# Performance work log

Measured on AMD Instinct MI355X. Metric: run time of the kernel, lower is better.

## Reference

```python
import jax, jax.numpy as jnp
import numpy as np

INV_SQRT2 = 0.7071067811865476  # pywt haar: cA=(x0+x1)/sqrt2, cD=(x0-x1)/sqrt2


def haar_dwt2(x):
    # x: (..., H, W) with even H, W. Matches pywt.dwt2 (cA, (cH, cV, cD))
    # keys: cH='da' (detail along rows), cV='ad', cD='dd'.
    aw = (x[..., ::2] + x[..., 1::2]) * INV_SQRT2   # low-pass along W
    dw = (x[..., ::2] - x[..., 1::2]) * INV_SQRT2   # high-pass along W
    LL = (aw[..., ::2, :] + aw[..., 1::2, :]) * INV_SQRT2
    LH = (aw[..., ::2, :] - aw[..., 1::2, :]) * INV_SQRT2  # cH
    HL = (dw[..., ::2, :] + dw[..., 1::2, :]) * INV_SQRT2  # cV
    HH = (dw[..., ::2, :] - dw[..., 1::2, :]) * INV_SQRT2  # cD
    return LL, LH, HL, HH


def _interleave_h(e, o):
    out_shape = e.shape[:-2] + (2 * e.shape[-2], e.shape[-1])
    return jnp.stack([e, o], axis=-2).reshape(out_shape)


def _interleave_w(e, o):
    out_shape = e.shape[:-1] + (2 * e.shape[-1],)
    return jnp.stack([e, o], axis=-1).reshape(out_shape)


def haar_idwt2(LL, LH, HL, HH):
    # exact inverse of haar_dwt2 (== pywt.idwt2 for haar, even sizes)
    aw = _interleave_h((LL + LH) * INV_SQRT2, (LL - LH) * INV_SQRT2)
    dw = _interleave_h((HL + HH) * INV_SQRT2, (HL - HH) * INV_SQRT2)
    return _interleave_w((aw + dw) * INV_SQRT2, (aw - dw) * INV_SQRT2)


def conv2d(x, w, b, stride, pad):
    y = jax.lax.conv_general_dilated(
        x, w, (stride, stride), [(pad, pad), (pad, pad)],
        dimension_numbers=('NCHW', 'OIHW', 'NCHW'))
    return y + b[None, :, None, None]


def conv_transpose2d(x, w, b, stride, pad):
    # torch ConvTranspose2d weight layout: (in, out, kH, kW)
    k = w.shape[2]
    wt = jnp.flip(jnp.transpose(w, (1, 0, 2, 3)), (2, 3))  # -> (out,in,kH,kW)
    p = k - 1 - pad
    y = jax.lax.conv_general_dilated(
        x, wt, (1, 1), [(p, p), (p, p)], lhs_dilation=(stride, stride),
        dimension_numbers=('NCHW', 'OIHW', 'NCHW'))
    return y + b[None, :, None, None]


def setup_inputs() -> dict:
    key = jax.random.key(0)
    k1, k2, k3 = jax.random.split(key, 3)
    B, C, H, W = 32, 3, 512, 512
    x = jax.random.normal(k1, (B, C, H, W), dtype=jnp.float32)
    # kaiming-style init for the small 9->9 convs
    down_w = jax.random.normal(k2, (9, 9, 3, 3), dtype=jnp.float32) * np.sqrt(2.0 / (9 * 9))
    down_b = jnp.zeros((9,), dtype=jnp.float32)
    up_w = jax.random.normal(k3, (9, 9, 4, 4), dtype=jnp.float32) * np.sqrt(2.0 / (9 * 16))
    up_b = jnp.zeros((9,), dtype=jnp.float32)
    return {"x": x, "down_w": down_w, "down_b": down_b, "up_w": up_w, "up_b": up_b}


def reference(x, down_w, down_b, up_w, up_b):
    B, C, H, W = x.shape
    # ---- encode ----
    LL1, LH1, HL1, HH1 = haar_dwt2(x)      # (B,C,H/2,W/2)
    LL2, LH2, HL2, HH2 = haar_dwt2(LL1)    # (B,C,H/4,W/4)
    level2 = jnp.stack([LL2, LH2, HL2, HH2], axis=2).reshape(B, C * 4, H // 4, W // 4)
    level1 = jnp.stack([LH1, HL1, HH1], axis=2).reshape(B, C * 3, H // 2, W // 2)
    level1_down = conv2d(level1, down_w, down_b, stride=2, pad=1)  # (B,9,H/4,W/4)
    z = jnp.concatenate([level2, level1_down], axis=1)             # (B,21,H/4,W/4)
    # ---- decode ----
    l2 = z[:, :4 * C].reshape(B, C, 4, H // 4, W // 4)
    l1 = conv_transpose2d(z[:, 4 * C:], up_w, up_b, stride=2, pad=1)
    l1 = l1.reshape(B, C, 3, H // 2, W // 2)
    LL1r = haar_idwt2(l2[:, :, 0], l2[:, :, 1], l2[:, :, 2], l2[:, :, 3])
    x_rec = haar_idwt2(LL1r, l1[:, :, 0], l1[:, :, 1], l1[:, :, 2])
    return x_rec
```

## Files before the change

kernel.cpp:

```cpp
#include <hip/hip_runtime.h>


#define BB 32

__global__ __launch_bounds__(256) void k0_rearrange(
    const float* __restrict__ dw, const float* __restrict__ uw,
    float* __restrict__ wd, float* __restrict__ wu)
{
    const int t = threadIdx.x;
    for (int i = t; i < 729; i += 256) {
        const int o    = i % 9;
        const int band = (i / 9) % 3;
        const int q    = (i / 27) % 3;
        const int a    = (i / 81) % 3;
        const int ch   = i / 243;
        wd[i] = 0.5f * dw[o * 81 + (ch * 3 + band) * 9 + a * 3 + q];
    }
    for (int i = t; i < 1296; i += 256) {
        const int o = i % 9; int r = i / 9;
        const int dj = r & 1; const int di = (r >> 1) & 1; r >>= 2;
        const int ct = r & 1; const int rt = (r >> 1) & 1; const int cin = r >> 2;
        wu[i] = uw[cin * 144 + o * 16 + (3 - di - 2 * rt) * 4 + (3 - dj - 2 * ct)];
    }
}

__global__ __launch_bounds__(256) void k1_dwt_down(
    const float* __restrict__ x,
    const float* __restrict__ wd,
    const float* __restrict__ db,
    float* __restrict__ LL1,
    float* __restrict__ y)
{
    const int t    = threadIdx.x;
    const int b    = blockIdx.x >> 6;
    const int tile = blockIdx.x & 63;
    const int I    = ((tile >> 3) << 4) + (t >> 4);
    const int J    = ((tile & 7) << 4) + (t & 15);

    float acc[9];
#pragma unroll
    for (int o = 0; o < 9; ++o) acc[o] = db[o];

    const bool jok  = (J > 0);
    const int  cofs = jok ? -2 : 0;

#pragma unroll
    for (int ch = 0; ch < 3; ++ch) {
        const float* xc  = x + ((size_t)b * 3 + ch) * 512 * 512;
        float*       llc = LL1 + ((size_t)b * 3 + ch) * 256 * 256;
#pragma unroll
        for (int a = 0; a < 3; ++a) {
            const int  r   = 2 * I - 1 + a;
            const bool rok = (r >= 0);
            const int  xr  = rok ? 2 * r : 0;
            const float* row0 = xc + (size_t)xr * 512 + 4 * J;
            const float* row1 = row0 + 512;

            float2 a0 = *reinterpret_cast<const float2*>(row0 + cofs);
            float2 a1 = *reinterpret_cast<const float2*>(row0);
            float2 a2 = *reinterpret_cast<const float2*>(row0 + 2);
            float2 b0 = *reinterpret_cast<const float2*>(row1 + cofs);
            float2 b1 = *reinterpret_cast<const float2*>(row1);
            float2 b2 = *reinterpret_cast<const float2*>(row1 + 2);
            if (!jok) { a0.x = a0.y = b0.x = b0.y = 0.f; }
            if (!rok) {
                a0.x = a0.y = a1.x = a1.y = a2.x = a2.y = 0.f;
                b0.x = b0.y = b1.x = b1.y = b2.x = b2.y = 0.f;
            }

            float lh[3], hl[3], hh[3], llq1, llq2;
            {
                const float s0 = a0.x + a0.y, d0 = a0.x - a0.y;
                const float s1 = b0.x + b0.y, d1 = b0.x - b0.y;
                lh[0] = s0 - s1; hl[0] = d0 + d1; hh[0] = d0 - d1;
            }
            {
                const float s0 = a1.x + a1.y, d0 = a1.x - a1.y;
                const float s1 = b1.x + b1.y, d1 = b1.x - b1.y;
                lh[1] = s0 - s1; hl[1] = d0 + d1; hh[1] = d0 - d1;
                llq1 = (s0 + s1) * 0.5f;
            }
            {
                const float s0 = a2.x + a2.y, d0 = a2.x - a2.y;
                const float s1 = b2.x + b2.y, d1 = b2.x - b2.y;
                lh[2] = s0 - s1; hl[2] = d0 + d1; hh[2] = d0 - d1;
                llq2 = (s0 + s1) * 0.5f;
            }

            if (a >= 1) {
                float2 llv; llv.x = llq1; llv.y = llq2;
                *reinterpret_cast<float2*>(llc + (size_t)r * 256 + 2 * J) = llv;
            }

            const float* wg = wd + ((ch * 3 + a) * 3) * 27;
#pragma unroll
            for (int q = 0; q < 3; ++q) {
                const float* w0 = wg + q * 27;
#pragma unroll
                for (int o = 0; o < 9; ++o) acc[o] += lh[q] * w0[o];
#pragma unroll
                for (int o = 0; o < 9; ++o) acc[o] += hl[q] * w0[9 + o];
#pragma unroll
                for (int o = 0; o < 9; ++o) acc[o] += hh[q] * w0[18 + o];
            }
        }
    }

#pragma unroll
    for (int o = 0; o < 9; ++o)
        y[(((size_t)b * 9 + o) * 128 + I) * 128 + J] = acc[o];
}

__global__ __launch_bounds__(256, 4) void k2_up_idwt(
    const float* __restrict__ yg,
    const float* __restrict__ wu,
    const float* __restrict__ ub,
    const float* __restrict__ LL1,
    float* __restrict__ out)
{
    __shared__ float ysh[9][18][19];

    const int t    = threadIdx.x;
    const int b    = blockIdx.x >> 6;
    const int tile = blockIdx.x & 63;
    const int r0   = (tile >> 3) << 5;
    const int c0   = (tile & 7) << 5;
    const int p0   = (r0 >> 1) - 1;
    const int q0   = (c0 >> 1) - 1;

    for (int item = t; item < 9 * 324; item += 256) {
        const int cin = item / 324;
        int rem       = item - cin * 324;
        const int lp  = rem / 18;
        const int lq  = rem - lp * 18;
        const int p   = p0 + lp, q = q0 + lq;
        float v = 0.f;
        if (p >= 0 && p < 128 && q >= 0 && q < 128)
            v = yg[(((size_t)b * 9 + cin) * 128 + p) * 128 + q];
        ysh[cin][lp][lq] = v;
    }
    __syncthreads();

    const int i2 = t >> 4;
    const int j2 = t & 15;

    float acc[2][2][9];
#pragma unroll
    for (int di = 0; di < 2; ++di)
#pragma unroll
        for (int dj = 0; dj < 2; ++dj)
#pragma unroll
            for (int o = 0; o < 9; ++o) acc[di][dj][o] = ub[o];

    for (int cin = 0; cin < 9; ++cin) {
        float yv[3][3];
#pragma unroll
        for (int r = 0; r < 3; ++r)
#pragma unroll
            for (int c = 0; c < 3; ++c)
                yv[r][c] = ysh[cin][i2 + r][j2 + c];
        const float* wc = wu + cin * 144;
#pragma unroll
        for (int rt = 0; rt < 2; ++rt)
#pragma unroll
            for (int ct = 0; ct < 2; ++ct) {
                const float* wg = wc + (rt * 2 + ct) * 36;
#pragma unroll
                for (int di = 0; di < 2; ++di)
#pragma unroll
                    for (int dj = 0; dj < 2; ++dj) {
                        const float vv = yv[di + rt][dj + ct];
                        const float* w9 = wg + (di * 2 + dj) * 9;
#pragma unroll
                        for (int o = 0; o < 9; ++o)
                            acc[di][dj][o] += vv * w9[o];
                    }
            }
    }

#pragma unroll
    for (int cc = 0; cc < 3; ++cc) {
#pragma unroll
        for (int di = 0; di < 2; ++di) {
            const int I = r0 + 2 * i2 + di;
            const int J = c0 + 2 * j2;
            const float2 llv = *reinterpret_cast<const float2*>(
                LL1 + (((size_t)b * 3 + cc) * 256 + I) * 256 + J);
            float4 top, bot;
            {
                const float ll = llv.x;
                const float lh = acc[di][0][cc * 3 + 0];
                const float hl = acc[di][0][cc * 3 + 1];
                const float hh = acc[di][0][cc * 3 + 2];
                const float e0 = ll + lh, od0 = ll - lh;
                const float e1 = hl + hh, od1 = hl - hh;
                top.x = (e0 + e1) * 0.5f; top.y = (e0 - e1) * 0.5f;
                bot.x = (od0 + od1) * 0.5f; bot.y = (od0 - od1) * 0.5f;
            }
            {
                const float ll = llv.y;
                const float lh = acc[di][1][cc * 3 + 0];
                const float hl = acc[di][1][cc * 3 + 1];
                const float hh = acc[di][1][cc * 3 + 2];
                const float e0 = ll + lh, od0 = ll - lh;
                const float e1 = hl + hh, od1 = hl - hh;
                top.z = (e0 + e1) * 0.5f; top.w = (e0 - e1) * 0.5f;
                bot.z = (od0 + od1) * 0.5f; bot.w = (od0 - od1) * 0.5f;
            }
            float* op = out + (((size_t)b * 3 + cc) * 512 + 2 * I) * 512 + 2 * J;
            *reinterpret_cast<float4*>(op) = top;
            *reinterpret_cast<float4*>(op + 512) = bot;
        }
    }
}

extern "C" void kernel_launch(void* const* d_in, const int* in_sizes, int n_in,
                              void* d_out, int out_size, void* d_ws, size_t ws_size,
                              hipStream_t stream) {
    const float* x  = (const float*)d_in[0];
    const float* dw = (const float*)d_in[1];
    const float* db = (const float*)d_in[2];
    const float* uw = (const float*)d_in[3];
    const float* ub = (const float*)d_in[4];
    float* outp = (float*)d_out;

    float* wsf = (float*)d_ws;
    float* wd  = wsf;
    float* wu  = wsf + 768;
    float* LL1 = wsf + 2304;
    float* y   = LL1 + (size_t)BB * 3 * 256 * 256;

    k0_rearrange<<<dim3(1), dim3(256), 0, stream>>>(dw, uw, wd, wu);
    k1_dwt_down<<<dim3(BB * 64), dim3(256), 0, stream>>>(x, wd, db, LL1, y);
    k2_up_idwt<<<dim3(BB * 64), dim3(256), 0, stream>>>(y, wu, ub, LL1, outp);
}
```

Measured before the change: 94.09 us.

## Stage input tile with halo in shared memory for DWT+downconv kernel

The first fused kernel now loads each channel's 66x68 input tile (including halo) into LDS with coalesced float4 loads, then each thread reads its 2x6 patch from shared memory instead of issuing overlapping float2 global loads. This removes redundant global reads of halo rows and columns and improves load coalescing. It adds block-level syncs per channel and about 18KB of LDS per block, which may lower occupancy.

```diff
diff --git a/kernel.cpp b/kernel.cpp
--- a/kernel.cpp
+++ b/kernel.cpp
@@ -31,68 +31,77 @@
     float* __restrict__ LL1,
     float* __restrict__ y)
 {
+    __shared__ float xs[66][68];
+
     const int t    = threadIdx.x;
     const int b    = blockIdx.x >> 6;
     const int tile = blockIdx.x & 63;
-    const int I    = ((tile >> 3) << 4) + (t >> 4);
-    const int J    = ((tile & 7) << 4) + (t & 15);
+    const int i0   = (tile >> 3) << 4;
+    const int j0   = (tile & 7) << 4;
+    const int ti   = t >> 4;
+    const int tj   = t & 15;
+    const int I    = i0 + ti;
+    const int J    = j0 + tj;
+
+    const int gr0 = 4 * i0 - 2;
+    const int gc0 = 4 * j0 - 4;
 
     float acc[9];
 #pragma unroll
     for (int o = 0; o < 9; ++o) acc[o] = db[o];
 
-    const bool jok  = (J > 0);
-    const int  cofs = jok ? -2 : 0;
-
-#pragma unroll
     for (int ch = 0; ch < 3; ++ch) {
-        const float* xc  = x + ((size_t)b * 3 + ch) * 512 * 512;
-        float*       llc = LL1 + ((size_t)b * 3 + ch) * 256 * 256;
+        const float* xc = x + ((size_t)b * 3 + ch) * 512 * 512;
+
+        if (ch) __syncthreads();
+        for (int idx = t; idx < 1122; idx += 256) {
+            const int lr = idx / 17;
+            const int f4 = idx - lr * 17;
+            const int gr = gr0 + lr;
+            float4 v = make_float4(0.f, 0.f, 0.f, 0.f);
+            if (gr >= 0 && !(f4 == 0 && j0 == 0))
+                v = *reinterpret_cast<const float4*>(xc + (size_t)gr * 512 + gc0 + 4 * f4);
+            *reinterpret_cast<float4*>(&xs[lr][4 * f4]) = v;
+        }
+        __syncthreads();
+
+        const float* wch = wd + ch * 243;
+        float* llc = LL1 + ((size_t)b * 3 + ch) * 256 * 256;
 #pragma unroll
         for (int a = 0; a < 3; ++a) {
-            const int  r   = 2 * I - 1 + a;
-            const bool rok = (r >= 0);
-            const int  xr  = rok ? 2 * r : 0;
-            const float* row0 = xc + (size_t)xr * 512 + 4 * J;
-            const float* row1 = row0 + 512;
-
-            float2 a0 = *reinterpret_cast<const float2*>(row0 + cofs);
-            float2 a1 = *reinterpret_cast<const float2*>(row0);
-            float2 a2 = *reinterpret_cast<const float2*>(row0 + 2);
-            float2 b0 = *reinterpret_cast<const float2*>(row1 + cofs);
-            float2 b1 = *reinterpret_cast<const float2*>(row1);
-            float2 b2 = *reinterpret_cast<const float2*>(row1 + 2);
-            if (!jok) { a0.x = a0.y = b0.x = b0.y = 0.f; }
-            if (!rok) {
-                a0.x = a0.y = a1.x = a1.y = a2.x = a2.y = 0.f;
-                b0.x = b0.y = b1.x = b1.y = b2.x = b2.y = 0.f;
-            }
-
-            float lh[3], hl[3], hh[3], llq1, llq2;
-            {
-                const float s0 = a0.x + a0.y, d0 = a0.x - a0.y;
-                const float s1 = b0.x + b0.y, d1 = b0.x - b0.y;
+            float2 p[2][3];
+#pragma unroll
+            for (int rr = 0; rr < 2; ++rr)
+#pragma unroll
+                for (int k = 0; k < 3; ++k)
+                    p[rr][k] = *reinterpret_cast<const float2*>(
+                        &xs[4 * ti + 2 * a + rr][4 * tj + 2 + 2 * k]);
+
+            float lh[3], hl[3], hh[3], llv1, llv2;
+            {
+                const float s0 = p[0][0].x + p[0][0].y, d0 = p[0][0].x - p[0][0].y;
+                const float s1 = p[1][0].x + p[1][0].y, d1 = p[1][0].x - p[1][0].y;
                 lh[0] = s0 - s1; hl[0] = d0 + d1; hh[0] = d0 - d1;
             }
             {
-                const float s0 = a1.x + a1.y, d0 = a1.x - a1.y;
-                const float s1 = b1.x + b1.y, d1 = b1.x - b1.y;
+                const float s0 = p[0][1].x + p[0][1].y, d0 = p[0][1].x - p[0][1].y;
+                const float s1 = p[1][1].x + p[1][1].y, d1 = p[1][1].x - p[1][1].y;
                 lh[1] = s0 - s1; hl[1] = d0 + d1; hh[1] = d0 - d1;
-                llq1 = (s0 + s1) * 0.5f;
-            }
-            {
-                const float s0 = a2.x + a2.y, d0 = a2.x - a2.y;
-                const float s1 = b2.x + b2.y, d1 = b2.x - b2.y;
+                llv1 = (s0 + s1) * 0.5f;
+            }
+            {
+                const float s0 = p[0][2].x + p[0][2].y, d0 = p[0][2].x - p[0][2].y;
+                const float s1 = p[1][2].x + p[1][2].y, d1 = p[1][2].x - p[1][2].y;
                 lh[2] = s0 - s1; hl[2] = d0 + d1; hh[2] = d0 - d1;
-                llq2 = (s0 + s1) * 0.5f;
+                llv2 = (s0 + s1) * 0.5f;
             }
 
             if (a >= 1) {
-                float2 llv; llv.x = llq1; llv.y = llq2;
-                *reinterpret_cast<float2*>(llc + (size_t)r * 256 + 2 * J) = llv;
-            }
-
-            const float* wg = wd + ((ch * 3 + a) * 3) * 27;
+                float2 w2; w2.x = llv1; w2.y = llv2;
+                *reinterpret_cast<float2*>(llc + (size_t)(2 * I - 1 + a) * 256 + 2 * J) = w2;
+            }
+
+            const float* wg = wch + a * 81;
 #pragma unroll
             for (int q = 0; q < 3; ++q) {
                 const float* w0 = wg + q * 27;
```

Measured after the change: 102.5 us. 1.09x slower.

## Restructure downsample kernel so each wave computes two output rows with row reuse

Applied to the files above, without the earlier changes.

The DWT+stride-2 conv kernel is reorganized so each wavefront handles a half-row strip and computes two adjacent output rows, loading 5 input row-pairs instead of 6 (overlapping halo rows reused). Loads become float4 plus a float2 halo per row instead of three float2s, and block IDs are swizzled across batches. This targets redundant global reads of the overlapping rows and wider memory transactions, at the cost of more registers per thread (two accumulator sets) and fewer blocks.

```diff
diff --git a/kernel.cpp b/kernel.cpp
--- a/kernel.cpp
+++ b/kernel.cpp
@@ -24,7 +24,7 @@
     }
 }
 
-__global__ __launch_bounds__(256) void k1_dwt_down(
+__global__ __launch_bounds__(256, 4) void k1_sweep(
     const float* __restrict__ x,
     const float* __restrict__ wd,
     const float* __restrict__ db,
@@ -32,83 +32,102 @@
     float* __restrict__ y)
 {
     const int t    = threadIdx.x;
-    const int b    = blockIdx.x >> 6;
-    const int tile = blockIdx.x & 63;
-    const int I    = ((tile >> 3) << 4) + (t >> 4);
-    const int J    = ((tile & 7) << 4) + (t & 15);
-
-    float acc[9];
-#pragma unroll
-    for (int o = 0; o < 9; ++o) acc[o] = db[o];
-
-    const bool jok  = (J > 0);
-    const int  cofs = jok ? -2 : 0;
+    const int w    = t >> 6;
+    const int l    = t & 63;
+    const int bid  = blockIdx.x;
+    const int swz  = (bid & 7) * 128 + (bid >> 3);
+    const int W    = swz * 4 + w;
+    const int b    = W >> 7;
+    const int rem  = W & 127;
+    const int half = rem & 1;
+    const int s    = rem >> 1;
+    const int c0   = 256 * half;
+    const int xcl  = c0 + 4 * l;
+    const bool lok = !(half == 0 && l == 0);
+    const int  xc2 = lok ? (xcl - 2) : 0;
+
+    float acc[2][9];
+#pragma unroll
+    for (int m = 0; m < 2; ++m)
+#pragma unroll
+        for (int o = 0; o < 9; ++o) acc[m][o] = db[o];
 
 #pragma unroll
     for (int ch = 0; ch < 3; ++ch) {
-        const float* xc  = x + ((size_t)b * 3 + ch) * 512 * 512;
-        float*       llc = LL1 + ((size_t)b * 3 + ch) * 256 * 256;
-#pragma unroll
-        for (int a = 0; a < 3; ++a) {
-            const int  r   = 2 * I - 1 + a;
+        const float* xc  = x + ((size_t)b * 3 + ch) * (512 * 512);
+        float*       llc = LL1 + ((size_t)b * 3 + ch) * (256 * 256);
+        const float* wch = wd + ch * 243;
+
+#pragma unroll
+        for (int rr = 0; rr < 5; ++rr) {
+            const int  r   = 4 * s - 1 + rr;
             const bool rok = (r >= 0);
             const int  xr  = rok ? 2 * r : 0;
-            const float* row0 = xc + (size_t)xr * 512 + 4 * J;
-            const float* row1 = row0 + 512;
-
-            float2 a0 = *reinterpret_cast<const float2*>(row0 + cofs);
-            float2 a1 = *reinterpret_cast<const float2*>(row0);
-            float2 a2 = *reinterpret_cast<const float2*>(row0 + 2);
-            float2 b0 = *reinterpret_cast<const float2*>(row1 + cofs);
-            float2 b1 = *reinterpret_cast<const float2*>(row1);
-            float2 b2 = *reinterpret_cast<const float2*>(row1 + 2);
-            if (!jok) { a0.x = a0.y = b0.x = b0.y = 0.f; }
+            const float* p0 = xc + (size_t)xr * 512;
+            const float* p1 = p0 + 512;
+
+            float4 A  = *reinterpret_cast<const float4*>(p0 + xcl);
+            float2 Ae = *reinterpret_cast<const float2*>(p0 + xc2);
+            float4 Bv = *reinterpret_cast<const float4*>(p1 + xcl);
+            float2 Be = *reinterpret_cast<const float2*>(p1 + xc2);
             if (!rok) {
-                a0.x = a0.y = a1.x = a1.y = a2.x = a2.y = 0.f;
-                b0.x = b0.y = b1.x = b1.y = b2.x = b2.y = 0.f;
-            }
-
-            float lh[3], hl[3], hh[3], llq1, llq2;
-            {
-                const float s0 = a0.x + a0.y, d0 = a0.x - a0.y;
-                const float s1 = b0.x + b0.y, d1 = b0.x - b0.y;
+                A.x = A.y = A.z = A.w = 0.f; Bv.x = Bv.y = Bv.z = Bv.w = 0.f;
+                Ae.x = Ae.y = 0.f; Be.x = Be.y = 0.f;
+            }
+            if (!lok) { Ae.x = Ae.y = 0.f; Be.x = Be.y = 0.f; }
+
+            float lh[3], hl[3], hh[3], ll0, ll1;
+            {
+                const float s0 = Ae.x + Ae.y, d0 = Ae.x - Ae.y;
+                const float s1 = Be.x + Be.y, d1 = Be.x - Be.y;
                 lh[0] = s0 - s1; hl[0] = d0 + d1; hh[0] = d0 - d1;
             }
             {
-                const float s0 = a1.x + a1.y, d0 = a1.x - a1.y;
-                const float s1 = b1.x + b1.y, d1 = b1.x - b1.y;
+                const float s0 = A.x + A.y, d0 = A.x - A.y;
+                const float s1 = Bv.x + Bv.y, d1 = Bv.x - Bv.y;
                 lh[1] = s0 - s1; hl[1] = d0 + d1; hh[1] = d0 - d1;
-                llq1 = (s0 + s1) * 0.5f;
-            }
-            {
-                const float s0 = a2.x + a2.y, d0 = a2.x - a2.y;
-                const float s1 = b2.x + b2.y, d1 = b2.x - b2.y;
+                ll0 = (s0 + s1) * 0.5f;
+            }
+            {
+                const float s0 = A.z + A.w, d0 = A.z - A.w;
+                const float s1 = Bv.z + Bv.w, d1 = Bv.z - Bv.w;
                 lh[2] = s0 - s1; hl[2] = d0 + d1; hh[2] = d0 - d1;
-                llq2 = (s0 + s1) * 0.5f;
-            }
-
-            if (a >= 1) {
-                float2 llv; llv.x = llq1; llv.y = llq2;
-                *reinterpret_cast<float2*>(llc + (size_t)r * 256 + 2 * J) = llv;
-            }
-
-            const float* wg = wd + ((ch * 3 + a) * 3) * 27;
-#pragma unroll
-            for (int q = 0; q < 3; ++q) {
-                const float* w0 = wg + q * 27;
-#pragma unroll
-                for (int o = 0; o < 9; ++o) acc[o] += lh[q] * w0[o];
-#pragma unroll
-                for (int o = 0; o < 9; ++o) acc[o] += hl[q] * w0[9 + o];
-#pragma unroll
-                for (int o = 0; o < 9; ++o) acc[o] += hh[q] * w0[18 + o];
+                ll1 = (s0 + s1) * 0.5f;
+            }
+
+            if (rr >= 1) {
+                float2 v; v.x = ll0; v.y = ll1;
+                *reinterpret_cast<float2*>(
+                    llc + (size_t)r * 256 + 128 * half + 2 * l) = v;
+            }
+
+#pragma unroll
+            for (int m = 0; m < 2; ++m) {
+                const int a = rr - 2 * m;
+                if (a >= 0 && a <= 2) {
+                    const float* wg = wch + a * 81;
+#pragma unroll
+                    for (int q = 0; q < 3; ++q) {
+                        const float* w0 = wg + q * 27;
+                        const float vlh = lh[q], vhl = hl[q], vhh = hh[q];
+#pragma unroll
+                        for (int o = 0; o < 9; ++o) acc[m][o] += vlh * w0[o];
+#pragma unroll
+                        for (int o = 0; o < 9; ++o) acc[m][o] += vhl * w0[9 + o];
+#pragma unroll
+                        for (int o = 0; o < 9; ++o) acc[m][o] += vhh * w0[18 + o];
+                    }
+                }
             }
         }
     }
 
-#pragma unroll
-    for (int o = 0; o < 9; ++o)
-        y[(((size_t)b * 9 + o) * 128 + I) * 128 + J] = acc[o];
+    const int J = 64 * half + l;
+#pragma unroll
+    for (int m = 0; m < 2; ++m)
+#pragma unroll
+        for (int o = 0; o < 9; ++o)
+            y[(((size_t)b * 9 + o) * 128 + (2 * s + m)) * 128 + J] = acc[m][o];
 }
 
 __global__ __launch_bounds__(256, 4) void k2_up_idwt(
@@ -231,6 +250,6 @@
     float* y   = LL1 + (size_t)BB * 3 * 256 * 256;
 
     k0_rearrange<<<dim3(1), dim3(256), 0, stream>>>(dw, uw, wd, wu);
-    k1_dwt_down<<<dim3(BB * 64), dim3(256), 0, stream>>>(x, wd, db, LL1, y);
+    k1_sweep<<<dim3(1024), dim3(256), 0, stream>>>(x, wd, db, LL1, y);
     k2_up_idwt<<<dim3(BB * 64), dim3(256), 0, stream>>>(y, wu, ub, LL1, outp);
 }
```

Measured after the change: 187.5 us. +99.3%, slower.
